# Performance work log

Hardware: AMD Instinct MI355X
Metric: run time of the kernel (lower is better)

The kernel has to match this reference:

```python
import jax, jax.numpy as jnp
import numpy as np

TEMPERATURE = 0.1
EPS = 1e-8  # torch cosine_similarity default eps


def _similarity_matrix(left, right):
    # C[i, j] = cosine_similarity(left[i], right[j]) with torch-style eps clamp
    ln = jnp.linalg.norm(left, axis=-1)   # [B]
    rn = jnp.linalg.norm(right, axis=-1)  # [B]
    dots = left @ right.T                 # [B, B]
    denom = jnp.maximum(ln[:, None] * rn[None, :], EPS)
    cos = dots / denom
    # Original builds only the strict upper triangle + diagonal of C, then
    # mirrors the upper triangle: S = triu(C, 1) + diag(C) + triu(C, 1).T
    upper = jnp.triu(cos, k=1)
    return upper + jnp.diag(jnp.diag(cos)) + upper.T


def reference(left_features, right_features):
    sims = _similarity_matrix(left_features, right_features) / TEMPERATURE
    # cross_entropy(sims, eye) == mean_i( -log_softmax(sims)[i, i] )
    logp = jax.nn.log_softmax(sims, axis=-1)
    return -jnp.mean(jnp.diagonal(logp))


def setup_inputs() -> dict:
    key = jax.random.key(0)
    k1, k2 = jax.random.split(key)
    B, D = 4096, 1024
    return {
        "left_features": jax.random.normal(k1, (B, D), dtype=jnp.float32),
        "right_features": jax.random.normal(k2, (B, D), dtype=jnp.float32),
    }
```

## Files before the change

### kernel.cpp

```cpp
#include <hip/hip_runtime.h>

typedef unsigned short u16;
typedef __bf16 bf16x8 __attribute__((ext_vector_type(8)));
typedef float f32x4 __attribute__((ext_vector_type(4)));

#define B_DIM 4096
#define D_DIM 1024
#define TT    32

#define GLOAD_LDS16(g, l)                                            \
    __builtin_amdgcn_global_load_lds(                                \
        (const __attribute__((address_space(1))) void*)(g),          \
        (__attribute__((address_space(3))) void*)(l), 16, 0, 0)

__device__ inline u16 f2bf(float f) {
    union { float f; unsigned u; } x; x.f = f;
    unsigned u = x.u;
    return (u16)((u + 0x7fffu + ((u >> 16) & 1u)) >> 16);
}

__device__ inline float wave_reduce_sum(float v) {
    #pragma unroll
    for (int off = 32; off > 0; off >>= 1) v += __shfl_down(v, off);
    return v;
}

__global__ __launch_bounds__(256) void norm_convert_kernel(
        const float* __restrict__ L, const float* __restrict__ R,
        u16* __restrict__ Lbf, u16* __restrict__ Rbf,
        float* __restrict__ ln, float* __restrict__ rn) {
    const int wave = threadIdx.x >> 6;
    const int lane = threadIdx.x & 63;
    int g = blockIdx.x * 4 + wave;
    const float* in; u16* outb; float* nout; int row;
    if (g < B_DIM) { in = L; outb = Lbf; nout = ln; row = g; }
    else           { in = R; outb = Rbf; nout = rn; row = g - B_DIM; }

    const float4* r4 = reinterpret_cast<const float4*>(in + (size_t)row * D_DIM);
    ushort4* o4 = reinterpret_cast<ushort4*>(outb + (size_t)row * D_DIM);
    float ss = 0.f;
    #pragma unroll
    for (int c = 0; c < 4; ++c) {
        float4 v = r4[lane + 64 * c];
        ss += v.x * v.x + v.y * v.y + v.z * v.z + v.w * v.w;
        ushort4 o;
        o.x = f2bf(v.x); o.y = f2bf(v.y); o.z = f2bf(v.z); o.w = f2bf(v.w);
        o4[lane + 64 * c] = o;
    }
    #pragma unroll
    for (int off = 32; off > 0; off >>= 1) ss += __shfl_xor(ss, off);
    if (lane == 0) nout[row] = sqrtf(ss);
}

__global__ __launch_bounds__(256) void gemm_fused_kernel(
        const u16* __restrict__ Lbf, const u16* __restrict__ Rbf,
        const float* __restrict__ ln, const float* __restrict__ rn,
        float* __restrict__ rowsum, float* __restrict__ diag) {
    __shared__ __align__(16) u16 Ls[2][128 * 64];
    __shared__ __align__(16) u16 Rs[2][128 * 64];

    int b = (int)blockIdx.x;
    int ti = 0;
    while (b >= TT - ti) { b -= TT - ti; ++ti; }
    const int tj = ti + b;
    const int brow = ti * 128;
    const int bcol = tj * 128;
    const bool diagblk = (ti == tj);

    const int tid  = threadIdx.x;
    const int lane = tid & 63;
    const int wave = tid >> 6;
    const int wr   = wave >> 1;
    const int wc   = wave & 1;
    const int fr   = lane & 15;

    const int l8 = lane >> 3;
    const int c8 = lane & 7;
    size_t gA[4], gB[4];
    int ldsOff[4];
    #pragma unroll
    for (int s = 0; s < 4; ++s) {
        int row = (wave * 4 + s) * 8 + l8;
        int chunk = c8 ^ (row & 7);
        gA[s] = (size_t)(brow + row) * D_DIM + chunk * 8;
        gB[s] = (size_t)(bcol + row) * D_DIM + chunk * 8;
        ldsOff[s] = (wave * 4 + s) * 512;
    }

#define STAGE(buf, k0)                                               \
    do {                                                             \
        _Pragma("unroll")                                            \
        for (int s = 0; s < 4; ++s) {                                \
            GLOAD_LDS16(Lbf + gA[s] + (k0), &Ls[buf][ldsOff[s]]);    \
            GLOAD_LDS16(Rbf + gB[s] + (k0), &Rs[buf][ldsOff[s]]);    \
        }                                                            \
    } while (0)

    f32x4 acc[4][4] = {};

#define COMPUTE(buf)                                                  \
    do {                                                              \
        _Pragma("unroll")                                             \
        for (int kk = 0; kk < 2; ++kk) {                              \
            bf16x8 af[4], bfr[4];                                     \
            _Pragma("unroll")                                         \
            for (int m = 0; m < 4; ++m) {                             \
                int row = wr * 64 + m * 16 + fr;                      \
                int cs = ((kk << 2) | (lane >> 4)) ^ (row & 7);       \
                af[m] = *reinterpret_cast<const bf16x8*>(             \
                    &Ls[buf][row * 64 + cs * 8]);                     \
            }                                                         \
            _Pragma("unroll")                                         \
            for (int n = 0; n < 4; ++n) {                             \
                int row = wc * 64 + n * 16 + fr;                      \
                int cs = ((kk << 2) | (lane >> 4)) ^ (row & 7);       \
                bfr[n] = *reinterpret_cast<const bf16x8*>(            \
                    &Rs[buf][row * 64 + cs * 8]);                     \
            }                                                         \
            _Pragma("unroll")                                         \
            for (int m = 0; m < 4; ++m)                               \
                _Pragma("unroll")                                     \
                for (int n = 0; n < 4; ++n)                           \
                    acc[m][n] = __builtin_amdgcn_mfma_f32_16x16x32_bf16( \
                        af[m], bfr[n], acc[m][n], 0, 0, 0);           \
        }                                                             \
    } while (0)

    STAGE(0, 0);
    __syncthreads();

    int cur = 0;
    for (int t = 0; t < 15; ++t) {
        STAGE(cur ^ 1, (t + 1) * 64);
        COMPUTE(cur);
        __syncthreads();
        cur ^= 1;
    }
    COMPUTE(cur);

    const int fcol  = lane & 15;
    const int frow0 = (lane >> 4) * 4;

    float rnj[4];
    #pragma unroll
    for (int n = 0; n < 4; ++n)
        rnj[n] = rn[bcol + wc * 64 + n * 16 + fcol];

    float colacc[4] = {0.f, 0.f, 0.f, 0.f};

    #pragma unroll
    for (int m = 0; m < 4; ++m) {
        #pragma unroll
        for (int r = 0; r < 4; ++r) {
            const int i = brow + wr * 64 + m * 16 + frow0 + r;
            const float lni = ln[i];
            float rowacc = 0.f;
            #pragma unroll
            for (int n = 0; n < 4; ++n) {
                const int j = bcol + wc * 64 + n * 16 + fcol;
                const float denom = fmaxf(lni * rnj[n], 1e-8f);
                const float v = acc[m][n][r] * 10.0f / denom;
                if (diagblk && i == j) diag[i] = v;
                const float e = __expf(v);
                if (i <= j) rowacc += e;
                if (i < j)  colacc[n] += e;
            }
            rowacc += __shfl_xor(rowacc, 1);
            rowacc += __shfl_xor(rowacc, 2);
            rowacc += __shfl_xor(rowacc, 4);
            rowacc += __shfl_xor(rowacc, 8);
            if (fcol == 0) atomicAdd(&rowsum[i], rowacc);
        }
    }
    #pragma unroll
    for (int n = 0; n < 4; ++n) {
        float c = colacc[n];
        c += __shfl_xor(c, 16);
        c += __shfl_xor(c, 32);
        if (lane < 16) {
            const int j = bcol + wc * 64 + n * 16 + fcol;
            atomicAdd(&rowsum[j], c);
        }
    }
#undef STAGE
#undef COMPUTE
}

__global__ __launch_bounds__(1024) void final_loss_kernel(
        const float* __restrict__ rowsum, const float* __restrict__ diag,
        float* __restrict__ out) {
    float s = 0.f;
    for (int i = threadIdx.x; i < B_DIM; i += 1024)
        s += logf(rowsum[i]) - diag[i];
    __shared__ float red[16];
    float w = wave_reduce_sum(s);
    if ((threadIdx.x & 63) == 0) red[threadIdx.x >> 6] = w;
    __syncthreads();
    if (threadIdx.x == 0) {
        float tot = 0.f;
        #pragma unroll
        for (int k = 0; k < 16; ++k) tot += red[k];
        out[0] = tot / (float)B_DIM;
    }
}

extern "C" void kernel_launch(void* const* d_in, const int* in_sizes, int n_in,
                              void* d_out, int out_size, void* d_ws, size_t ws_size,
                              hipStream_t stream) {
    const float* L = (const float*)d_in[0];
    const float* R = (const float*)d_in[1];

    char* ws = (char*)d_ws;
    size_t o = 0;
    u16* Lbf   = (u16*)(ws + o);   o += (size_t)B_DIM * D_DIM * sizeof(u16);
    u16* Rbf   = (u16*)(ws + o);   o += (size_t)B_DIM * D_DIM * sizeof(u16);
    float* ln  = (float*)(ws + o); o += (size_t)B_DIM * sizeof(float);
    float* rn  = (float*)(ws + o); o += (size_t)B_DIM * sizeof(float);
    float* rs  = (float*)(ws + o); o += (size_t)B_DIM * sizeof(float);
    float* dg  = (float*)(ws + o); o += (size_t)B_DIM * sizeof(float);

    hipMemsetAsync(rs, 0, B_DIM * sizeof(float), stream);

    norm_convert_kernel<<<2 * B_DIM / 4, 256, 0, stream>>>(L, R, Lbf, Rbf, ln, rn);

    const int nblocks = TT * (TT + 1) / 2;
    gemm_fused_kernel<<<nblocks, 256, 0, stream>>>(Lbf, Rbf, ln, rn, rs, dg);

    final_loss_kernel<<<1, 1024, 0, stream>>>(rs, dg, (float*)d_out);
}
```

Before: 138.5 us.

## Overlap LDS staging with fine-grained vmcnt waits, swizzle block order, fold memset

```diff
diff --git a/kernel.cpp b/kernel.cpp
--- a/kernel.cpp
+++ b/kernel.cpp
@@ -7,6 +7,7 @@
 #define B_DIM 4096
 #define D_DIM 1024
 #define TT    32
+#define NT    16
 
 #define GLOAD_LDS16(g, l)                                            \
     __builtin_amdgcn_global_load_lds(                                \
@@ -28,7 +29,13 @@
 __global__ __launch_bounds__(256) void norm_convert_kernel(
         const float* __restrict__ L, const float* __restrict__ R,
         u16* __restrict__ Lbf, u16* __restrict__ Rbf,
-        float* __restrict__ ln, float* __restrict__ rn) {
+        float* __restrict__ ln, float* __restrict__ rn,
+        float* __restrict__ rowsum) {
+    if (blockIdx.x == 0) {
+        #pragma unroll
+        for (int i = 0; i < B_DIM / 256; ++i)
+            rowsum[threadIdx.x + i * 256] = 0.f;
+    }
     const int wave = threadIdx.x >> 6;
     const int lane = threadIdx.x & 63;
     int g = blockIdx.x * 4 + wave;
@@ -59,7 +66,9 @@
     __shared__ __align__(16) u16 Ls[2][128 * 64];
     __shared__ __align__(16) u16 Rs[2][128 * 64];
 
-    int b = (int)blockIdx.x;
+    int bid = (int)blockIdx.x;
+    int swz = (bid & 7) * 66 + (bid >> 3);
+    int b = swz;
     int ti = 0;
     while (b >= TT - ti) { b -= TT - ti; ++ti; }
     const int tj = ti + b;
@@ -127,16 +136,22 @@
     } while (0)
 
     STAGE(0, 0);
-    __syncthreads();
 
     int cur = 0;
-    for (int t = 0; t < 15; ++t) {
-        STAGE(cur ^ 1, (t + 1) * 64);
+    for (int t = 0; t < NT; ++t) {
+        if (t + 1 < NT) {
+            STAGE(cur ^ 1, (t + 1) * 64);
+            asm volatile("s_waitcnt vmcnt(8)" ::: "memory");
+        } else {
+            asm volatile("s_waitcnt vmcnt(0)" ::: "memory");
+        }
+        __builtin_amdgcn_s_barrier();
+        asm volatile("" ::: "memory");
         COMPUTE(cur);
-        __syncthreads();
+        asm volatile("" ::: "memory");
+        __builtin_amdgcn_s_barrier();
         cur ^= 1;
     }
-    COMPUTE(cur);
 
     const int fcol  = lane & 15;
     const int frow0 = (lane >> 4) * 4;
@@ -219,9 +234,7 @@
     float* rs  = (float*)(ws + o); o += (size_t)B_DIM * sizeof(float);
     float* dg  = (float*)(ws + o); o += (size_t)B_DIM * sizeof(float);
 
-    hipMemsetAsync(rs, 0, B_DIM * sizeof(float), stream);
-
-    norm_convert_kernel<<<2 * B_DIM / 4, 256, 0, stream>>>(L, R, Lbf, Rbf, ln, rn);
+    norm_convert_kernel<<<2 * B_DIM / 4, 256, 0, stream>>>(L, R, Lbf, Rbf, ln, rn, rs);
 
     const int nblocks = TT * (TT + 1) / 2;
     gemm_fused_kernel<<<nblocks, 256, 0, stream>>>(Lbf, Rbf, ln, rn, rs, dg);
```

Result: faster. 131.7 us (-4.9%).

## Fuse fp32-to-bf16 conversion and norms into GEMM, replace atomics with partial slots

Applied to the files above, without the earlier changes.

```diff
diff --git a/kernel.cpp b/kernel.cpp
--- a/kernel.cpp
+++ b/kernel.cpp
@@ -1,70 +1,29 @@
 #include <hip/hip_runtime.h>
 
 typedef unsigned short u16;
+typedef __bf16 bf16_t;
 typedef __bf16 bf16x8 __attribute__((ext_vector_type(8)));
 typedef float f32x4 __attribute__((ext_vector_type(4)));
 
 #define B_DIM 4096
 #define D_DIM 1024
 #define TT    32
-
-#define GLOAD_LDS16(g, l)                                            \
-    __builtin_amdgcn_global_load_lds(                                \
-        (const __attribute__((address_space(1))) void*)(g),          \
-        (__attribute__((address_space(3))) void*)(l), 16, 0, 0)
-
-__device__ inline u16 f2bf(float f) {
-    union { float f; unsigned u; } x; x.f = f;
-    unsigned u = x.u;
-    return (u16)((u + 0x7fffu + ((u >> 16) & 1u)) >> 16);
-}
-
-__device__ inline float wave_reduce_sum(float v) {
-    #pragma unroll
-    for (int off = 32; off > 0; off >>= 1) v += __shfl_down(v, off);
-    return v;
-}
-
-__global__ __launch_bounds__(256) void norm_convert_kernel(
-        const float* __restrict__ L, const float* __restrict__ R,
-        u16* __restrict__ Lbf, u16* __restrict__ Rbf,
-        float* __restrict__ ln, float* __restrict__ rn) {
-    const int wave = threadIdx.x >> 6;
-    const int lane = threadIdx.x & 63;
-    int g = blockIdx.x * 4 + wave;
-    const float* in; u16* outb; float* nout; int row;
-    if (g < B_DIM) { in = L; outb = Lbf; nout = ln; row = g; }
-    else           { in = R; outb = Rbf; nout = rn; row = g - B_DIM; }
-
-    const float4* r4 = reinterpret_cast<const float4*>(in + (size_t)row * D_DIM);
-    ushort4* o4 = reinterpret_cast<ushort4*>(outb + (size_t)row * D_DIM);
-    float ss = 0.f;
-    #pragma unroll
-    for (int c = 0; c < 4; ++c) {
-        float4 v = r4[lane + 64 * c];
-        ss += v.x * v.x + v.y * v.y + v.z * v.z + v.w * v.w;
-        ushort4 o;
-        o.x = f2bf(v.x); o.y = f2bf(v.y); o.z = f2bf(v.z); o.w = f2bf(v.w);
-        o4[lane + 64 * c] = o;
-    }
-    #pragma unroll
-    for (int off = 32; off > 0; off >>= 1) ss += __shfl_xor(ss, off);
-    if (lane == 0) nout[row] = sqrtf(ss);
-}
-
-__global__ __launch_bounds__(256) void gemm_fused_kernel(
-        const u16* __restrict__ Lbf, const u16* __restrict__ Rbf,
-        const float* __restrict__ ln, const float* __restrict__ rn,
-        float* __restrict__ rowsum, float* __restrict__ diag) {
+#define NT    16
+#define NSLOT 66
+
+__global__ __launch_bounds__(256, 2) void gemm_fused_kernel(
+        const float* __restrict__ Lf, const float* __restrict__ Rf,
+        float* __restrict__ part, float* __restrict__ diag) {
     __shared__ __align__(16) u16 Ls[2][128 * 64];
     __shared__ __align__(16) u16 Rs[2][128 * 64];
-
-    int b = (int)blockIdx.x;
-    int ti = 0;
+    __shared__ float nA[128], nB[128];
+
+    int bid = (int)blockIdx.x;
+    int swz = (bid & 7) * 66 + (bid >> 3);
+    int b = swz, ti = 0;
     while (b >= TT - ti) { b -= TT - ti; ++ti; }
     const int tj = ti + b;
-    const int brow = ti * 128;
-    const int bcol = tj * 128;
+    const int brow = ti * 128, bcol = tj * 128;
     const bool diagblk = (ti == tj);
 
     const int tid  = threadIdx.x;
@@ -74,69 +33,109 @@
     const int wc   = wave & 1;
     const int fr   = lane & 15;
 
-    const int l8 = lane >> 3;
-    const int c8 = lane & 7;
-    size_t gA[4], gB[4];
-    int ldsOff[4];
-    #pragma unroll
-    for (int s = 0; s < 4; ++s) {
-        int row = (wave * 4 + s) * 8 + l8;
-        int chunk = c8 ^ (row & 7);
-        gA[s] = (size_t)(brow + row) * D_DIM + chunk * 8;
-        gB[s] = (size_t)(bcol + row) * D_DIM + chunk * 8;
-        ldsOff[s] = (wave * 4 + s) * 512;
-    }
-
-#define STAGE(buf, k0)                                               \
-    do {                                                             \
-        _Pragma("unroll")                                            \
-        for (int s = 0; s < 4; ++s) {                                \
-            GLOAD_LDS16(Lbf + gA[s] + (k0), &Ls[buf][ldsOff[s]]);    \
-            GLOAD_LDS16(Rbf + gB[s] + (k0), &Rs[buf][ldsOff[s]]);    \
-        }                                                            \
+    const int srow = tid >> 3;
+    const int sc   = tid & 7;
+    const int swcs = sc ^ (srow & 7);
+
+    const float* pA = Lf + (size_t)brow * D_DIM;
+    const float* pB = Rf + (size_t)bcol * D_DIM;
+
+    float4 ga[8], gb[8];
+    float ssA[4] = {0.f, 0.f, 0.f, 0.f};
+    float ssB[4] = {0.f, 0.f, 0.f, 0.f};
+    f32x4 acc[4][4] = {};
+
+#define LOADREGS(k0)                                                         \
+    do {                                                                     \
+        _Pragma("unroll")                                                    \
+        for (int p = 0; p < 4; ++p) {                                        \
+            const float* a = pA + (size_t)(p * 32 + srow) * D_DIM + (k0) + sc * 8; \
+            ga[2 * p]     = *reinterpret_cast<const float4*>(a);             \
+            ga[2 * p + 1] = *reinterpret_cast<const float4*>(a + 4);         \
+            const float* bp = pB + (size_t)(p * 32 + srow) * D_DIM + (k0) + sc * 8; \
+            gb[2 * p]     = *reinterpret_cast<const float4*>(bp);            \
+            gb[2 * p + 1] = *reinterpret_cast<const float4*>(bp + 4);        \
+        }                                                                    \
     } while (0)
 
-    f32x4 acc[4][4] = {};
-
-#define COMPUTE(buf)                                                  \
-    do {                                                              \
-        _Pragma("unroll")                                             \
-        for (int kk = 0; kk < 2; ++kk) {                              \
-            bf16x8 af[4], bfr[4];                                     \
-            _Pragma("unroll")                                         \
-            for (int m = 0; m < 4; ++m) {                             \
-                int row = wr * 64 + m * 16 + fr;                      \
-                int cs = ((kk << 2) | (lane >> 4)) ^ (row & 7);       \
-                af[m] = *reinterpret_cast<const bf16x8*>(             \
-                    &Ls[buf][row * 64 + cs * 8]);                     \
-            }                                                         \
-            _Pragma("unroll")                                         \
-            for (int n = 0; n < 4; ++n) {                             \
-                int row = wc * 64 + n * 16 + fr;                      \
-                int cs = ((kk << 2) | (lane >> 4)) ^ (row & 7);       \
-                bfr[n] = *reinterpret_cast<const bf16x8*>(            \
-                    &Rs[buf][row * 64 + cs * 8]);                     \
-            }                                                         \
-            _Pragma("unroll")                                         \
-            for (int m = 0; m < 4; ++m)                               \
-                _Pragma("unroll")                                     \
-                for (int n = 0; n < 4; ++n)                           \
-                    acc[m][n] = __builtin_amdgcn_mfma_f32_16x16x32_bf16( \
-                        af[m], bfr[n], acc[m][n], 0, 0, 0);           \
-        }                                                             \
+#define CVTWRITE(buf)                                                        \
+    do {                                                                     \
+        _Pragma("unroll")                                                    \
+        for (int p = 0; p < 4; ++p) {                                        \
+            float4 x = ga[2 * p], y = ga[2 * p + 1];                         \
+            ssA[p] += x.x * x.x + x.y * x.y + x.z * x.z + x.w * x.w          \
+                    + y.x * y.x + y.y * y.y + y.z * y.z + y.w * y.w;         \
+            bf16x8 v;                                                        \
+            v[0] = (bf16_t)x.x; v[1] = (bf16_t)x.y;                          \
+            v[2] = (bf16_t)x.z; v[3] = (bf16_t)x.w;                          \
+            v[4] = (bf16_t)y.x; v[5] = (bf16_t)y.y;                          \
+            v[6] = (bf16_t)y.z; v[7] = (bf16_t)y.w;                          \
+            *reinterpret_cast<bf16x8*>(                                      \
+                &Ls[buf][(p * 32 + srow) * 64 + swcs * 8]) = v;              \
+            x = gb[2 * p]; y = gb[2 * p + 1];                                \
+            ssB[p] += x.x * x.x + x.y * x.y + x.z * x.z + x.w * x.w          \
+                    + y.x * y.x + y.y * y.y + y.z * y.z + y.w * y.w;         \
+            v[0] = (bf16_t)x.x; v[1] = (bf16_t)x.y;                          \
+            v[2] = (bf16_t)x.z; v[3] = (bf16_t)x.w;                          \
+            v[4] = (bf16_t)y.x; v[5] = (bf16_t)y.y;                          \
+            v[6] = (bf16_t)y.z; v[7] = (bf16_t)y.w;                          \
+            *reinterpret_cast<bf16x8*>(                                      \
+                &Rs[buf][(p * 32 + srow) * 64 + swcs * 8]) = v;              \
+        }                                                                    \
     } while (0)
 
-    STAGE(0, 0);
+#define COMPUTE(buf)                                                         \
+    do {                                                                     \
+        _Pragma("unroll")                                                    \
+        for (int kk = 0; kk < 2; ++kk) {                                     \
+            bf16x8 af[4], bfr[4];                                            \
+            _Pragma("unroll")                                                \
+            for (int m = 0; m < 4; ++m) {                                    \
+                int row = wr * 64 + m * 16 + fr;                             \
+                int cs = ((kk << 2) | (lane >> 4)) ^ (row & 7);              \
+                af[m] = *reinterpret_cast<const bf16x8*>(                    \
+                    &Ls[buf][row * 64 + cs * 8]);                            \
+            }                                                                \
+            _Pragma("unroll")                                                \
+            for (int n = 0; n < 4; ++n) {                                    \
+                int row = wc * 64 + n * 16 + fr;                             \
+                int cs = ((kk << 2) | (lane >> 4)) ^ (row & 7);              \
+                bfr[n] = *reinterpret_cast<const bf16x8*>(                   \
+                    &Rs[buf][row * 64 + cs * 8]);                            \
+            }                                                                \
+            _Pragma("unroll")                                                \
+            for (int m = 0; m < 4; ++m)                                      \
+                _Pragma("unroll")                                            \
+                for (int n = 0; n < 4; ++n)                                  \
+                    acc[m][n] = __builtin_amdgcn_mfma_f32_16x16x32_bf16(     \
+                        af[m], bfr[n], acc[m][n], 0, 0, 0);                  \
+        }                                                                    \
+    } while (0)
+
+    LOADREGS(0);
+    CVTWRITE(0);
     __syncthreads();
 
     int cur = 0;
-    for (int t = 0; t < 15; ++t) {
-        STAGE(cur ^ 1, (t + 1) * 64);
+    for (int t = 0; t < NT; ++t) {
+        if (t + 1 < NT) LOADREGS((t + 1) * 64);
         COMPUTE(cur);
+        if (t + 1 < NT) CVTWRITE(cur ^ 1);
         __syncthreads();
         cur ^= 1;
     }
-    COMPUTE(cur);
+
+    #pragma unroll
+    for (int p = 0; p < 4; ++p) {
+        float sa = ssA[p], sb = ssB[p];
+        sa += __shfl_xor(sa, 1); sa += __shfl_xor(sa, 2); sa += __shfl_xor(sa, 4);
+        sb += __shfl_xor(sb, 1); sb += __shfl_xor(sb, 2); sb += __shfl_xor(sb, 4);
+        if (sc == 0) {
+            nA[p * 32 + srow] = sqrtf(sa);
+            nB[p * 32 + srow] = sqrtf(sb);
+        }
+    }
+    __syncthreads();
 
     const int fcol  = lane & 15;
     const int frow0 = (lane >> 4) * 4;
@@ -144,7 +143,7 @@
     float rnj[4];
     #pragma unroll
     for (int n = 0; n < 4; ++n)
-        rnj[n] = rn[bcol + wc * 64 + n * 16 + fcol];
+        rnj[n] = nB[wc * 64 + n * 16 + fcol];
 
     float colacc[4] = {0.f, 0.f, 0.f, 0.f};
 
@@ -152,8 +151,9 @@
     for (int m = 0; m < 4; ++m) {
         #pragma unroll
         for (int r = 0; r < 4; ++r) {
-            const int i = brow + wr * 64 + m * 16 + frow0 + r;
-            const float lni = ln[i];
+            const int li = wr * 64 + m * 16 + frow0 + r;
+            const int i  = brow + li;
+            const float lni = nA[li];
             float rowacc = 0.f;
             #pragma unroll
             for (int n = 0; n < 4; ++n) {
@@ -169,7 +169,7 @@
             rowacc += __shfl_xor(rowacc, 2);
             rowacc += __shfl_xor(rowacc, 4);
             rowacc += __shfl_xor(rowacc, 8);
-            if (fcol == 0) atomicAdd(&rowsum[i], rowacc);
+            if (fcol == 0) part[(size_t)(2 * tj + wc) * B_DIM + i] = rowacc;
         }
     }
     #pragma unroll
@@ -179,22 +179,30 @@
         c += __shfl_xor(c, 32);
         if (lane < 16) {
             const int j = bcol + wc * 64 + n * 16 + fcol;
-            atomicAdd(&rowsum[j], c);
+            const int slot = diagblk ? (64 + wr) : (2 * ti + wr);
+            part[(size_t)slot * B_DIM + j] = c;
         }
     }
-#undef STAGE
+#undef LOADREGS
+#undef CVTWRITE
 #undef COMPUTE
 }
 
 __global__ __launch_bounds__(1024) void final_loss_kernel(
-        const float* __restrict__ rowsum, const float* __restrict__ diag,
+        const float* __restrict__ part, const float* __restrict__ diag,
         float* __restrict__ out) {
     float s = 0.f;
-    for (int i = threadIdx.x; i < B_DIM; i += 1024)
-        s += logf(rowsum[i]) - diag[i];
+    for (int i = threadIdx.x; i < B_DIM; i += 1024) {
+        float rs = 0.f;
+        #pragma unroll
+        for (int k = 0; k < NSLOT; ++k)
+            rs += part[(size_t)k * B_DIM + i];
+        s += logf(rs) - diag[i];
+    }
     __shared__ float red[16];
-    float w = wave_reduce_sum(s);
-    if ((threadIdx.x & 63) == 0) red[threadIdx.x >> 6] = w;
+    #pragma unroll
+    for (int off = 32; off > 0; off >>= 1) s += __shfl_down(s, off);
+    if ((threadIdx.x & 63) == 0) red[threadIdx.x >> 6] = s;
     __syncthreads();
     if (threadIdx.x == 0) {
         float tot = 0.f;
@@ -211,20 +219,10 @@
     const float* R = (const float*)d_in[1];
 
     char* ws = (char*)d_ws;
-    size_t o = 0;
-    u16* Lbf   = (u16*)(ws + o);   o += (size_t)B_DIM * D_DIM * sizeof(u16);
-    u16* Rbf   = (u16*)(ws + o);   o += (size_t)B_DIM * D_DIM * sizeof(u16);
-    float* ln  = (float*)(ws + o); o += (size_t)B_DIM * sizeof(float);
-    float* rn  = (float*)(ws + o); o += (size_t)B_DIM * sizeof(float);
-    float* rs  = (float*)(ws + o); o += (size_t)B_DIM * sizeof(float);
-    float* dg  = (float*)(ws + o); o += (size_t)B_DIM * sizeof(float);
-
-    hipMemsetAsync(rs, 0, B_DIM * sizeof(float), stream);
-
-    norm_convert_kernel<<<2 * B_DIM / 4, 256, 0, stream>>>(L, R, Lbf, Rbf, ln, rn);
+    float* part = (float*)ws;
+    float* diag = (float*)(ws + (size_t)NSLOT * B_DIM * sizeof(float));
 
     const int nblocks = TT * (TT + 1) / 2;
-    gemm_fused_kernel<<<nblocks, 256, 0, stream>>>(Lbf, Rbf, ln, rn, rs, dg);
-
-    final_loss_kernel<<<1, 1024, 0, stream>>>(rs, dg, (float*)d_out);
+    gemm_fused_kernel<<<nblocks, 256, 0, stream>>>(L, R, part, diag);
+    final_loss_kernel<<<1, 1024, 0, stream>>>(part, diag, (float*)d_out);
 }
```

After: 207.8 us. 50.0% more time.
